# Performance work log

Hardware: AMD Instinct MI355X
Metric: run time of the kernel (lower is better)

Reference implementation:

```python
import jax, jax.numpy as jnp
import numpy as np

B, T, S, D, H, DK, DV = 4, 2048, 2048, 1024, 16, 64, 64


def setup_inputs() -> dict:
    key = jax.random.key(0)
    ks = jax.random.split(key, 12)
    sq = 1.0 / np.sqrt(D)
    return {
        "query": jax.random.normal(ks[0], (B, T, D), jnp.float32),
        "value": jax.random.normal(ks[1], (B, S, D), jnp.float32),
        "mask": jnp.ones((B, T, S), dtype=bool),
        "Wq": jax.random.normal(ks[2], (D, H, DK), jnp.float32) * sq,
        "bq": jnp.zeros((H, DK), jnp.float32),
        "Wk": jax.random.normal(ks[3], (D, H, DK), jnp.float32) * sq,
        "bk": jnp.zeros((H, DK), jnp.float32),
        "Wv": jax.random.normal(ks[4], (D, H, DV), jnp.float32) * sq,
        "bv": jnp.zeros((H, DV), jnp.float32),
        "Wo": jax.random.normal(ks[5], (H, DV, D), jnp.float32) * (1.0 / np.sqrt(H * DV)),
        "bo": jnp.zeros((D,), jnp.float32),
    }


def reference(query, value, mask, Wq, bq, Wk, bk, Wv, bv, Wo, bo):
    # key input defaults to value when only [query, value] is given
    q = jnp.einsum("btd,dhk->bthk", query, Wq) + bq  # [B,T,H,DK]
    k = jnp.einsum("bsd,dhk->bshk", value, Wk) + bk  # [B,S,H,DK]
    v = jnp.einsum("bsd,dhv->bshv", value, Wv) + bv  # [B,S,H,DV]
    # dot_product_equation 'aecd,abcd->acbe': scores[b,h,t,s]
    scores = jnp.einsum("bshk,bthk->bhts", k, q) * (1.0 / np.sqrt(DK))
    # MaskedSoftmax: mask [B,T,S] expanded at axis 1 -> [B,1,T,S]
    adder = (1.0 - mask[:, None, :, :].astype(scores.dtype)) * -10000.0
    probs = jax.nn.softmax(scores + adder, axis=-1)
    # combine_equation 'acbe,aecd->abcd'
    attn = jnp.einsum("bhts,bshv->bthv", probs, v)  # [B,T,H,DV]
    out = jnp.einsum("bthv,hvd->btd", attn, Wo) + bo  # [B,T,D]
    return out
```

## Files before the change

kernel.cpp:

```cpp
#include <hip/hip_runtime.h>

typedef __bf16 bf16x8 __attribute__((ext_vector_type(8)));
typedef __bf16 bf16x4 __attribute__((ext_vector_type(4)));
typedef float  f32x4  __attribute__((ext_vector_type(4)));
typedef int    i32x4  __attribute__((ext_vector_type(4)));

typedef __attribute__((address_space(1))) unsigned int as1_u32;
typedef __attribute__((address_space(3))) unsigned int as3_u32;

#define DEVI __device__ __forceinline__

DEVI unsigned short f2bf(float f) {
    union { float f; unsigned u; } v; v.f = f;
    unsigned r = (v.u + 0x7fffu + ((v.u >> 16) & 1u)) >> 16;
    return (unsigned short)r;
}

DEVI void gload16(const void* g, void* l) {
    __builtin_amdgcn_global_load_lds((const as1_u32*)g, (as3_u32*)l, 16, 0, 0);
}

#define C_EXP 0.18033688011112042f
#define MASK_ADD (-14426.950408889634f)

__global__ __launch_bounds__(256) void cvt_kernel(const float* __restrict__ in,
                                                  unsigned short* __restrict__ out,
                                                  int n8) {
    const int stride = gridDim.x * 256;
    for (int idx = blockIdx.x * 256 + threadIdx.x; idx < n8; idx += stride) {
        const f32x4 a = *(const f32x4*)(in + (size_t)idx * 8);
        const f32x4 b = *(const f32x4*)(in + (size_t)idx * 8 + 4);
        union { bf16x4 v[2]; i32x4 q; } u;
        u.v[0] = __builtin_convertvector(a, bf16x4);
        u.v[1] = __builtin_convertvector(b, bf16x4);
        *(i32x4*)(out + (size_t)idx * 8) = u.q;
    }
}

__global__ __launch_bounds__(256) void wtrans_kernel(const float* __restrict__ W0,
                                                     const float* __restrict__ W1,
                                                     const float* __restrict__ W2,
                                                     const float* __restrict__ W3,
                                                     unsigned short* __restrict__ T0,
                                                     unsigned short* __restrict__ T1,
                                                     unsigned short* __restrict__ T2,
                                                     unsigned short* __restrict__ T3) {
    __shared__ float tile[64][65];
    const float* W;
    unsigned short* WT;
    float scale = 1.0f;
    switch (blockIdx.z) {
        case 0:  W = W0; WT = T0; scale = C_EXP; break;
        case 1:  W = W1; WT = T1; break;
        case 2:  W = W2; WT = T2; break;
        default: W = W3; WT = T3; break;
    }
    const int k0 = blockIdx.x * 64, n0 = blockIdx.y * 64;
    const int i = threadIdx.x;
    const int c4 = (i & 15) * 4, rbase = i >> 4;
    for (int rr = 0; rr < 4; ++rr) {
        const int kl = rbase + rr * 16;
        const float4 v = *(const float4*)(W + (size_t)(k0 + kl) * 1024 + n0 + c4);
        tile[kl][c4 + 0] = v.x; tile[kl][c4 + 1] = v.y;
        tile[kl][c4 + 2] = v.z; tile[kl][c4 + 3] = v.w;
    }
    __syncthreads();
    for (int rr = 0; rr < 4; ++rr) {
        const int nl = rbase + rr * 16;
        ushort4 o;
        o.x = f2bf(tile[c4 + 0][nl] * scale); o.y = f2bf(tile[c4 + 1][nl] * scale);
        o.z = f2bf(tile[c4 + 2][nl] * scale); o.w = f2bf(tile[c4 + 3][nl] * scale);
        *(ushort4*)(WT + (size_t)(n0 + nl) * 1024 + k0 + c4) = o;
    }
}

__global__ __launch_bounds__(256) void maskflag_kernel(const int* __restrict__ mask,
                                                       unsigned char* __restrict__ flags) {
    const int bid = blockIdx.x;
    const int b = bid >> 9, rem = bid & 511;
    const int tb = rem >> 5, si = rem & 31;
    const int i = threadIdx.x;
    const int t = tb * 128 + (i >> 1);
    const int s = si * 64 + (i & 1) * 32;
    const uint4* p = (const uint4*)(mask + ((size_t)(b * 2048 + t)) * 2048 + s);
    int ok = 1;
    #pragma unroll
    for (int u = 0; u < 8; ++u) {
        const uint4 a = p[u];
        ok &= (a.x != 0) & (a.y != 0) & (a.z != 0) & (a.w != 0);
    }
    int all = __syncthreads_and(ok);
    if (i == 0) flags[bid] = (unsigned char)all;
}

template <int MODE>
__global__ __launch_bounds__(256) void mm_kernel(const unsigned short* __restrict__ A,
                                                 const unsigned short* __restrict__ BT,
                                                 const float* __restrict__ bias,
                                                 float bscale,
                                                 void* __restrict__ Ov) {
    __shared__ __align__(16) unsigned short Ab[128 * 32];
    __shared__ __align__(16) unsigned short Bb[128 * 32];
    const int bid = blockIdx.x;
    const int xcd = bid & 7, jj = bid >> 3;
    const int n0 = (jj & 7) * 128;
    const int m0 = ((jj >> 3) * 8 + xcd) * 128;
    const int i = threadIdx.x, w = i >> 6, l = i & 63;
    const int wm = w >> 1, wn = w & 1;
    const int c = l & 15, g = l >> 4;
    const int rloc = l >> 2;
    const int schunk = ((l & 3) ^ ((l >> 3) & 3)) * 8;
    const int rs = (c >> 1) & 3;

    f32x4 acc[4][4] = {};

    const unsigned short* Asrc = A + (size_t)(m0 + w * 32 + rloc) * 1024 + schunk;
    const unsigned short* Bsrc = BT + (size_t)(n0 + w * 32 + rloc) * 1024 + schunk;
    unsigned short* AbBase = &Ab[(w * 32) * 32];
    unsigned short* BbBase = &Bb[(w * 32) * 32];

    for (int k0 = 0; k0 < 1024; k0 += 32) {
        gload16(Asrc + k0,             AbBase);
        gload16(Asrc + k0 + 16 * 1024, AbBase + 16 * 32);
        gload16(Bsrc + k0,             BbBase);
        gload16(Bsrc + k0 + 16 * 1024, BbBase + 16 * 32);
        __syncthreads();
        bf16x8 af[4], bfr[4];
        #pragma unroll
        for (int mf = 0; mf < 4; ++mf)
            af[mf] = *(const bf16x8*)&Ab[(wm * 64 + mf * 16 + c) * 32 + (g ^ rs) * 8];
        #pragma unroll
        for (int nf = 0; nf < 4; ++nf)
            bfr[nf] = *(const bf16x8*)&Bb[(wn * 64 + nf * 16 + c) * 32 + (g ^ rs) * 8];
        #pragma unroll
        for (int mf = 0; mf < 4; ++mf)
            #pragma unroll
            for (int nf = 0; nf < 4; ++nf)
                acc[mf][nf] = __builtin_amdgcn_mfma_f32_16x16x32_bf16(af[mf], bfr[nf], acc[mf][nf], 0, 0, 0);
        __syncthreads();
    }

    #pragma unroll
    for (int nf = 0; nf < 4; ++nf) {
        const int n = n0 + wn * 64 + nf * 16 + c;
        const float bv = bias[n] * bscale;
        const int h = n >> 6, cc = n & 63;
        #pragma unroll
        for (int mf = 0; mf < 4; ++mf) {
            const int mbase = m0 + wm * 64 + mf * 16 + g * 4;
            if (MODE == 0) {
                const int b = mbase >> 11, t = mbase & 2047;
                unsigned short* O = (unsigned short*)Ov;
                #pragma unroll
                for (int r = 0; r < 4; ++r)
                    O[(((size_t)(b * 16 + h)) * 2048 + t + r) * 64 + cc] = f2bf(acc[mf][nf][r] + bv);
            } else if (MODE == 1) {
                const int b = mbase >> 11, t = mbase & 2047;
                f32x4 v;
                #pragma unroll
                for (int r = 0; r < 4; ++r) v[r] = acc[mf][nf][r] + bv;
                bf16x4 pv = __builtin_convertvector(v, bf16x4);
                unsigned short* O = (unsigned short*)Ov;
                *(bf16x4*)(O + (((size_t)(b * 16 + h)) * 64 + cc) * 2048 + t) = pv;
            } else {
                float* O = (float*)Ov;
                #pragma unroll
                for (int r = 0; r < 4; ++r)
                    O[(size_t)(mbase + r) * 1024 + n] = acc[mf][nf][r] + bv;
            }
        }
    }
}

__global__ __launch_bounds__(256) void attn_kernel(const unsigned short* __restrict__ Qp,
                                                   const unsigned short* __restrict__ Kp,
                                                   const unsigned short* __restrict__ VTp,
                                                   const int* __restrict__ mask,
                                                   const unsigned char* __restrict__ flags,
                                                   unsigned short* __restrict__ attnb) {
    __shared__ __align__(16) unsigned short Kt[2][64 * 64];
    __shared__ __align__(16) unsigned short Vt[2][64 * 64];

    const int bid = blockIdx.x;
    const int xcd = bid & 7, jj = bid >> 3;
    const int bh = xcd * 8 + (jj >> 4);
    const int tb = jj & 15;
    const int b = bh >> 4, h = bh & 15;
    const int i = threadIdx.x, w = i >> 6, l = i & 63;
    const int c = l & 15, g = l >> 4;

    const unsigned short* Qb  = Qp  + (size_t)bh * 2048 * 64;
    const unsigned short* Kb  = Kp  + (size_t)bh * 2048 * 64;
    const unsigned short* VTb = VTp + (size_t)bh * 64 * 2048;

    const int twave = tb * 128 + w * 32;

    bf16x8 qf[2][2];
    #pragma unroll
    for (int tn = 0; tn < 2; ++tn)
        #pragma unroll
        for (int kq = 0; kq < 2; ++kq)
            qf[tn][kq] = *(const bf16x8*)(Qb + (size_t)(twave + tn * 16 + c) * 64 + kq * 32 + g * 8);

    f32x4 o[4][2] = {};
    f32x4 dacc[2] = {};

    bf16x8 ones8;
    #pragma unroll
    for (int j = 0; j < 8; ++j) ones8[j] = (__bf16)1.0f;

    int rrow[4], rswz[4];
    #pragma unroll
    for (int sm = 0; sm < 4; ++sm) {
        rrow[sm] = (sm >> 1) * 32 + (c >> 2) * 8 + (sm & 1) * 4 + (c & 3);
        rswz[sm] = (rrow[sm] ^ (rrow[sm] >> 2)) & 7;
    }
    int vswz[4];
    #pragma unroll
    for (int vm = 0; vm < 4; ++vm) {
        const int rv = vm * 16 + c;
        vswz[vm] = (rv ^ (rv >> 2)) & 7;
    }

    const int srow = l >> 3, sslot = l & 7;

    #pragma unroll
    for (int u = 0; u < 2; ++u) {
        const int row = w * 16 + u * 8 + srow;
        const int ch = sslot ^ ((row ^ (row >> 2)) & 7);
        gload16(Kb + (size_t)row * 64 + ch * 8, &Kt[0][(w * 16 + u * 8) * 64]);
        gload16(VTb + (size_t)row * 2048 + ch * 8, &Vt[0][(w * 16 + u * 8) * 64]);
    }
    __syncthreads();

    for (int it = 0; it < 32; ++it) {
        const int buf = it & 1;
        const int s0 = it * 64;

        if (it < 31) {
            const int s0n = s0 + 64;
            #pragma unroll
            for (int u = 0; u < 2; ++u) {
                const int row = w * 16 + u * 8 + srow;
                const int ch = sslot ^ ((row ^ (row >> 2)) & 7);
                gload16(Kb + (size_t)(s0n + row) * 64 + ch * 8, &Kt[buf ^ 1][(w * 16 + u * 8) * 64]);
                gload16(VTb + (size_t)row * 2048 + s0n + ch * 8, &Vt[buf ^ 1][(w * 16 + u * 8) * 64]);
            }
        }

        f32x4 sc[4][2] = {};
        #pragma unroll
        for (int sm = 0; sm < 4; ++sm)
            #pragma unroll
            for (int kq = 0; kq < 2; ++kq) {
                const bf16x8 kf = *(const bf16x8*)&Kt[buf][rrow[sm] * 64 + (((kq * 4 + g) ^ rswz[sm]) * 8)];
                #pragma unroll
                for (int tn = 0; tn < 2; ++tn)
                    sc[sm][tn] = __builtin_amdgcn_mfma_f32_16x16x32_bf16(kf, qf[tn][kq], sc[sm][tn], 0, 0, 0);
            }

        const int flg = flags[(b * 16 + tb) * 32 + it];
        if (!flg) {
            #pragma unroll
            for (int sm = 0; sm < 4; ++sm)
                #pragma unroll
                for (int tn = 0; tn < 2; ++tn)
                    #pragma unroll
                    for (int r = 0; r < 4; ++r) {
                        const int t = twave + tn * 16 + c;
                        const int s = s0 + (sm >> 1) * 32 + g * 8 + (sm & 1) * 4 + r;
                        if (mask[(size_t)(b * 2048 + t) * 2048 + s] == 0) sc[sm][tn][r] += MASK_ADD;
                    }
        }

        unsigned pk[4][2][2];
        #pragma unroll
        for (int sm = 0; sm < 4; ++sm)
            #pragma unroll
            for (int tn = 0; tn < 2; ++tn) {
                f32x4 p;
                #pragma unroll
                for (int r = 0; r < 4; ++r)
                    p[r] = __builtin_amdgcn_exp2f(sc[sm][tn][r]);
                union { bf16x4 v; unsigned d[2]; } u;
                u.v = __builtin_convertvector(p, bf16x4);
                pk[sm][tn][0] = u.d[0];
                pk[sm][tn][1] = u.d[1];
            }

        #pragma unroll
        for (int kv = 0; kv < 2; ++kv) {
            bf16x8 pa[2];
            #pragma unroll
            for (int tn = 0; tn < 2; ++tn) {
                union { i32x4 q; bf16x8 v; } pu;
                pu.q[0] = (int)pk[kv * 2][tn][0];
                pu.q[1] = (int)pk[kv * 2][tn][1];
                pu.q[2] = (int)pk[kv * 2 + 1][tn][0];
                pu.q[3] = (int)pk[kv * 2 + 1][tn][1];
                pa[tn] = pu.v;
            }
            #pragma unroll
            for (int tn = 0; tn < 2; ++tn)
                dacc[tn] = __builtin_amdgcn_mfma_f32_16x16x32_bf16(ones8, pa[tn], dacc[tn], 0, 0, 0);
            #pragma unroll
            for (int vm = 0; vm < 4; ++vm) {
                const bf16x8 vf = *(const bf16x8*)&Vt[buf][(vm * 16 + c) * 64 + (((kv * 4 + g) ^ vswz[vm]) * 8)];
                #pragma unroll
                for (int tn = 0; tn < 2; ++tn)
                    o[vm][tn] = __builtin_amdgcn_mfma_f32_16x16x32_bf16(vf, pa[tn], o[vm][tn], 0, 0, 0);
            }
        }

        __syncthreads();
    }

    float inv[2];
    #pragma unroll
    for (int tn = 0; tn < 2; ++tn) inv[tn] = 1.0f / dacc[tn][0];

    #pragma unroll
    for (int vm = 0; vm < 4; ++vm)
        #pragma unroll
        for (int tn = 0; tn < 2; ++tn) {
            const int t = twave + tn * 16 + c;
            f32x4 v4;
            #pragma unroll
            for (int r = 0; r < 4; ++r) v4[r] = o[vm][tn][r] * inv[tn];
            bf16x4 pv = __builtin_convertvector(v4, bf16x4);
            *(bf16x4*)(attnb + (size_t)(b * 2048 + t) * 1024 + h * 64 + vm * 16 + g * 4) = pv;
        }
}

extern "C" void kernel_launch(void* const* d_in, const int* in_sizes, int n_in,
                              void* d_out, int out_size, void* d_ws, size_t ws_size,
                              hipStream_t stream) {
    const float* query = (const float*)d_in[0];
    const float* value = (const float*)d_in[1];
    const int*   mask  = (const int*)d_in[2];
    const float* Wq = (const float*)d_in[3];
    const float* bq = (const float*)d_in[4];
    const float* Wk = (const float*)d_in[5];
    const float* bk = (const float*)d_in[6];
    const float* Wv = (const float*)d_in[7];
    const float* bv = (const float*)d_in[8];
    const float* Wo = (const float*)d_in[9];
    const float* bo = (const float*)d_in[10];

    char* ws = (char*)d_ws;
    unsigned short* WqT   = (unsigned short*)(ws + ((size_t)0  << 20));
    unsigned short* WkT   = (unsigned short*)(ws + ((size_t)2  << 20));
    unsigned short* WvT   = (unsigned short*)(ws + ((size_t)4  << 20));
    unsigned short* WoT   = (unsigned short*)(ws + ((size_t)6  << 20));
    unsigned char*  flags = (unsigned char*) (ws + ((size_t)8  << 20));
    unsigned short* CONV  = (unsigned short*)(ws + ((size_t)9  << 20));
    unsigned short* Qp    = (unsigned short*)(ws + ((size_t)25 << 20));
    unsigned short* Kp    = (unsigned short*)(ws + ((size_t)41 << 20));
    unsigned short* VTp   = (unsigned short*)(ws + ((size_t)57 << 20));

    const int n8 = 8192 * 1024 / 8;

    cvt_kernel<<<2048, 256, 0, stream>>>(value, CONV, n8);
    wtrans_kernel<<<dim3(16, 16, 4), 256, 0, stream>>>(Wq, Wk, Wv, Wo, WqT, WkT, WvT, WoT);
    maskflag_kernel<<<2048, 256, 0, stream>>>(mask, flags);
    mm_kernel<0><<<512, 256, 0, stream>>>(CONV, WkT, bk, 1.0f, Kp);
    mm_kernel<1><<<512, 256, 0, stream>>>(CONV, WvT, bv, 1.0f, VTp);

    cvt_kernel<<<2048, 256, 0, stream>>>(query, CONV, n8);
    mm_kernel<0><<<512, 256, 0, stream>>>(CONV, WqT, bq, C_EXP, Qp);

    attn_kernel<<<1024, 256, 0, stream>>>(Qp, Kp, VTp, mask, flags, CONV);

    mm_kernel<2><<<512, 256, 0, stream>>>(CONV, WoT, bo, 1.0f, (float*)d_out);
}
```

Measured before the change: 232.8 us.

## Halve attention query tile per wave, raise occupancy, pack mask flags into bitmasks

Each attention wave now handles 16 query rows instead of 32, so the grid doubles to 2048 blocks and launch bounds ask for 5 blocks per CU, cutting register pressure to allow more resident waves. Mask-all-ones flags become one 32-bit bitmask per (batch, 128-row block), set by atomicOr and read once per block with readfirstlane. A hipMemsetAsync clears the bitmask words before the mask pass. The change also adds s_setprio around the MFMA sections, advances the staging pointers incrementally, and unrolls the key loop by two. The cost is that each K/V tile staged in LDS now feeds half as many MFMAs, so global and LDS traffic per unit of compute doubles.

```diff
diff --git a/kernel.cpp b/kernel.cpp
--- a/kernel.cpp
+++ b/kernel.cpp
@@ -75,7 +75,7 @@
 }
 
 __global__ __launch_bounds__(256) void maskflag_kernel(const int* __restrict__ mask,
-                                                       unsigned char* __restrict__ flags) {
+                                                       unsigned* __restrict__ flagsW) {
     const int bid = blockIdx.x;
     const int b = bid >> 9, rem = bid & 511;
     const int tb = rem >> 5, si = rem & 31;
@@ -90,7 +90,7 @@
         ok &= (a.x != 0) & (a.y != 0) & (a.z != 0) & (a.w != 0);
     }
     int all = __syncthreads_and(ok);
-    if (i == 0) flags[bid] = (unsigned char)all;
+    if (i == 0 && !all) atomicOr(&flagsW[b * 16 + tb], 1u << si);
 }
 
 template <int MODE>
@@ -172,19 +172,19 @@
     }
 }
 
-__global__ __launch_bounds__(256) void attn_kernel(const unsigned short* __restrict__ Qp,
-                                                   const unsigned short* __restrict__ Kp,
-                                                   const unsigned short* __restrict__ VTp,
-                                                   const int* __restrict__ mask,
-                                                   const unsigned char* __restrict__ flags,
-                                                   unsigned short* __restrict__ attnb) {
+__global__ __launch_bounds__(256, 5) void attn_kernel(const unsigned short* __restrict__ Qp,
+                                                      const unsigned short* __restrict__ Kp,
+                                                      const unsigned short* __restrict__ VTp,
+                                                      const int* __restrict__ mask,
+                                                      const unsigned* __restrict__ flagsW,
+                                                      unsigned short* __restrict__ attnb) {
     __shared__ __align__(16) unsigned short Kt[2][64 * 64];
     __shared__ __align__(16) unsigned short Vt[2][64 * 64];
 
     const int bid = blockIdx.x;
     const int xcd = bid & 7, jj = bid >> 3;
-    const int bh = xcd * 8 + (jj >> 4);
-    const int tb = jj & 15;
+    const int bh = xcd * 8 + (jj >> 5);
+    const int tb = jj & 31;
     const int b = bh >> 4, h = bh & 15;
     const int i = threadIdx.x, w = i >> 6, l = i & 63;
     const int c = l & 15, g = l >> 4;
@@ -193,17 +193,17 @@
     const unsigned short* Kb  = Kp  + (size_t)bh * 2048 * 64;
     const unsigned short* VTb = VTp + (size_t)bh * 64 * 2048;
 
-    const int twave = tb * 128 + w * 32;
-
-    bf16x8 qf[2][2];
-    #pragma unroll
-    for (int tn = 0; tn < 2; ++tn)
-        #pragma unroll
-        for (int kq = 0; kq < 2; ++kq)
-            qf[tn][kq] = *(const bf16x8*)(Qb + (size_t)(twave + tn * 16 + c) * 64 + kq * 32 + g * 8);
-
-    f32x4 o[4][2] = {};
-    f32x4 dacc[2] = {};
+    const int twave = tb * 64 + w * 16;
+
+    const unsigned notall = __builtin_amdgcn_readfirstlane(flagsW[b * 16 + (tb >> 1)]);
+
+    bf16x8 qf[2];
+    #pragma unroll
+    for (int kq = 0; kq < 2; ++kq)
+        qf[kq] = *(const bf16x8*)(Qb + (size_t)(twave + c) * 64 + kq * 32 + g * 8);
+
+    f32x4 o[4] = {};
+    f32x4 dacc = {};
 
     bf16x8 ones8;
     #pragma unroll
@@ -224,112 +224,97 @@
 
     const int srow = l >> 3, sslot = l & 7;
 
+    const unsigned short* kstage[2];
+    const unsigned short* vstage[2];
     #pragma unroll
     for (int u = 0; u < 2; ++u) {
         const int row = w * 16 + u * 8 + srow;
         const int ch = sslot ^ ((row ^ (row >> 2)) & 7);
         gload16(Kb + (size_t)row * 64 + ch * 8, &Kt[0][(w * 16 + u * 8) * 64]);
         gload16(VTb + (size_t)row * 2048 + ch * 8, &Vt[0][(w * 16 + u * 8) * 64]);
+        kstage[u] = Kb + (size_t)(64 + row) * 64 + ch * 8;
+        vstage[u] = VTb + (size_t)row * 2048 + 64 + ch * 8;
     }
     __syncthreads();
 
+    #pragma unroll 2
     for (int it = 0; it < 32; ++it) {
         const int buf = it & 1;
         const int s0 = it * 64;
 
         if (it < 31) {
-            const int s0n = s0 + 64;
             #pragma unroll
             for (int u = 0; u < 2; ++u) {
-                const int row = w * 16 + u * 8 + srow;
-                const int ch = sslot ^ ((row ^ (row >> 2)) & 7);
-                gload16(Kb + (size_t)(s0n + row) * 64 + ch * 8, &Kt[buf ^ 1][(w * 16 + u * 8) * 64]);
-                gload16(VTb + (size_t)row * 2048 + s0n + ch * 8, &Vt[buf ^ 1][(w * 16 + u * 8) * 64]);
-            }
-        }
-
-        f32x4 sc[4][2] = {};
+                gload16(kstage[u], &Kt[buf ^ 1][(w * 16 + u * 8) * 64]);
+                gload16(vstage[u], &Vt[buf ^ 1][(w * 16 + u * 8) * 64]);
+                kstage[u] += 64 * 64;
+                vstage[u] += 64;
+            }
+        }
+
+        f32x4 sc[4] = {};
+        __builtin_amdgcn_s_setprio(1);
         #pragma unroll
         for (int sm = 0; sm < 4; ++sm)
             #pragma unroll
             for (int kq = 0; kq < 2; ++kq) {
                 const bf16x8 kf = *(const bf16x8*)&Kt[buf][rrow[sm] * 64 + (((kq * 4 + g) ^ rswz[sm]) * 8)];
-                #pragma unroll
-                for (int tn = 0; tn < 2; ++tn)
-                    sc[sm][tn] = __builtin_amdgcn_mfma_f32_16x16x32_bf16(kf, qf[tn][kq], sc[sm][tn], 0, 0, 0);
-            }
-
-        const int flg = flags[(b * 16 + tb) * 32 + it];
-        if (!flg) {
+                sc[sm] = __builtin_amdgcn_mfma_f32_16x16x32_bf16(kf, qf[kq], sc[sm], 0, 0, 0);
+            }
+        __builtin_amdgcn_s_setprio(0);
+
+        if (notall & (1u << it)) {
             #pragma unroll
             for (int sm = 0; sm < 4; ++sm)
                 #pragma unroll
-                for (int tn = 0; tn < 2; ++tn)
-                    #pragma unroll
-                    for (int r = 0; r < 4; ++r) {
-                        const int t = twave + tn * 16 + c;
-                        const int s = s0 + (sm >> 1) * 32 + g * 8 + (sm & 1) * 4 + r;
-                        if (mask[(size_t)(b * 2048 + t) * 2048 + s] == 0) sc[sm][tn][r] += MASK_ADD;
-                    }
-        }
-
-        unsigned pk[4][2][2];
-        #pragma unroll
-        for (int sm = 0; sm < 4; ++sm)
-            #pragma unroll
-            for (int tn = 0; tn < 2; ++tn) {
-                f32x4 p;
-                #pragma unroll
-                for (int r = 0; r < 4; ++r)
-                    p[r] = __builtin_amdgcn_exp2f(sc[sm][tn][r]);
-                union { bf16x4 v; unsigned d[2]; } u;
-                u.v = __builtin_convertvector(p, bf16x4);
-                pk[sm][tn][0] = u.d[0];
-                pk[sm][tn][1] = u.d[1];
-            }
-
+                for (int r = 0; r < 4; ++r) {
+                    const int t = twave + c;
+                    const int s = s0 + (sm >> 1) * 32 + g * 8 + (sm & 1) * 4 + r;
+                    if (mask[(size_t)(b * 2048 + t) * 2048 + s] == 0) sc[sm][r] += MASK_ADD;
+                }
+        }
+
+        bf16x8 pa[2];
         #pragma unroll
         for (int kv = 0; kv < 2; ++kv) {
-            bf16x8 pa[2];
-            #pragma unroll
-            for (int tn = 0; tn < 2; ++tn) {
-                union { i32x4 q; bf16x8 v; } pu;
-                pu.q[0] = (int)pk[kv * 2][tn][0];
-                pu.q[1] = (int)pk[kv * 2][tn][1];
-                pu.q[2] = (int)pk[kv * 2 + 1][tn][0];
-                pu.q[3] = (int)pk[kv * 2 + 1][tn][1];
-                pa[tn] = pu.v;
-            }
-            #pragma unroll
-            for (int tn = 0; tn < 2; ++tn)
-                dacc[tn] = __builtin_amdgcn_mfma_f32_16x16x32_bf16(ones8, pa[tn], dacc[tn], 0, 0, 0);
+            f32x4 p0, p1;
+            #pragma unroll
+            for (int r = 0; r < 4; ++r) {
+                p0[r] = __builtin_amdgcn_exp2f(sc[kv * 2][r]);
+                p1[r] = __builtin_amdgcn_exp2f(sc[kv * 2 + 1][r]);
+            }
+            union { struct { bf16x4 lo, hi; } h; bf16x8 v; } u;
+            u.h.lo = __builtin_convertvector(p0, bf16x4);
+            u.h.hi = __builtin_convertvector(p1, bf16x4);
+            pa[kv] = u.v;
+        }
+
+        __builtin_amdgcn_s_setprio(1);
+        #pragma unroll
+        for (int kv = 0; kv < 2; ++kv) {
+            dacc = __builtin_amdgcn_mfma_f32_16x16x32_bf16(ones8, pa[kv], dacc, 0, 0, 0);
             #pragma unroll
             for (int vm = 0; vm < 4; ++vm) {
                 const bf16x8 vf = *(const bf16x8*)&Vt[buf][(vm * 16 + c) * 64 + (((kv * 4 + g) ^ vswz[vm]) * 8)];
-                #pragma unroll
-                for (int tn = 0; tn < 2; ++tn)
-                    o[vm][tn] = __builtin_amdgcn_mfma_f32_16x16x32_bf16(vf, pa[tn], o[vm][tn], 0, 0, 0);
-            }
-        }
+                o[vm] = __builtin_amdgcn_mfma_f32_16x16x32_bf16(vf, pa[kv], o[vm], 0, 0, 0);
+            }
+        }
+        __builtin_amdgcn_s_setprio(0);
 
         __syncthreads();
     }
 
-    float inv[2];
-    #pragma unroll
-    for (int tn = 0; tn < 2; ++tn) inv[tn] = 1.0f / dacc[tn][0];
-
-    #pragma unroll
-    for (int vm = 0; vm < 4; ++vm)
-        #pragma unroll
-        for (int tn = 0; tn < 2; ++tn) {
-            const int t = twave + tn * 16 + c;
-            f32x4 v4;
-            #pragma unroll
-            for (int r = 0; r < 4; ++r) v4[r] = o[vm][tn][r] * inv[tn];
-            bf16x4 pv = __builtin_convertvector(v4, bf16x4);
-            *(bf16x4*)(attnb + (size_t)(b * 2048 + t) * 1024 + h * 64 + vm * 16 + g * 4) = pv;
-        }
+    const float inv = 1.0f / dacc[0];
+
+    const int t = twave + c;
+    #pragma unroll
+    for (int vm = 0; vm < 4; ++vm) {
+        f32x4 v4;
+        #pragma unroll
+        for (int r = 0; r < 4; ++r) v4[r] = o[vm][r] * inv;
+        bf16x4 pv = __builtin_convertvector(v4, bf16x4);
+        *(bf16x4*)(attnb + (size_t)(b * 2048 + t) * 1024 + h * 64 + vm * 16 + g * 4) = pv;
+    }
 }
 
 extern "C" void kernel_launch(void* const* d_in, const int* in_sizes, int n_in,
@@ -352,7 +337,7 @@
     unsigned short* WkT   = (unsigned short*)(ws + ((size_t)2  << 20));
     unsigned short* WvT   = (unsigned short*)(ws + ((size_t)4  << 20));
     unsigned short* WoT   = (unsigned short*)(ws + ((size_t)6  << 20));
-    unsigned char*  flags = (unsigned char*) (ws + ((size_t)8  << 20));
+    unsigned*       flagsW= (unsigned*)      (ws + ((size_t)8  << 20));
     unsigned short* CONV  = (unsigned short*)(ws + ((size_t)9  << 20));
     unsigned short* Qp    = (unsigned short*)(ws + ((size_t)25 << 20));
     unsigned short* Kp    = (unsigned short*)(ws + ((size_t)41 << 20));
@@ -360,16 +345,18 @@
 
     const int n8 = 8192 * 1024 / 8;
 
+    hipMemsetAsync(flagsW, 0, 64 * sizeof(unsigned), stream);
+
     cvt_kernel<<<2048, 256, 0, stream>>>(value, CONV, n8);
     wtrans_kernel<<<dim3(16, 16, 4), 256, 0, stream>>>(Wq, Wk, Wv, Wo, WqT, WkT, WvT, WoT);
-    maskflag_kernel<<<2048, 256, 0, stream>>>(mask, flags);
+    maskflag_kernel<<<2048, 256, 0, stream>>>(mask, flagsW);
     mm_kernel<0><<<512, 256, 0, stream>>>(CONV, WkT, bk, 1.0f, Kp);
     mm_kernel<1><<<512, 256, 0, stream>>>(CONV, WvT, bv, 1.0f, VTp);
 
     cvt_kernel<<<2048, 256, 0, stream>>>(query, CONV, n8);
     mm_kernel<0><<<512, 256, 0, stream>>>(CONV, WqT, bq, C_EXP, Qp);
 
-    attn_kernel<<<1024, 256, 0, stream>>>(Qp, Kp, VTp, mask, flags, CONV);
+    attn_kernel<<<2048, 256, 0, stream>>>(Qp, Kp, VTp, mask, flagsW, CONV);
 
     mm_kernel<2><<<512, 256, 0, stream>>>(CONV, WoT, bo, 1.0f, (float*)d_out);
 }
```

Result: faster. 224.2 us (-3.7%).
